# Performance work log

Measured on AMD Instinct MI355X. Metric: run time of the kernel, lower is better.

## Reference

```python
import jax, jax.numpy as jnp
import numpy as np

VOCAB = 256
UNITS = 512

def setup_inputs() -> dict:
    key = jax.random.key(0)
    ks = jax.random.split(key, 7)
    B, T = 64, 1024
    scale = 0.02
    return {
        "inputs": jax.random.randint(ks[0], (B, T), 0, VOCAB, dtype=jnp.int32),
        "emb": jax.random.normal(ks[1], (VOCAB, VOCAB), dtype=jnp.float32) * scale,
        "Wx": jax.random.normal(ks[2], (VOCAB, UNITS), dtype=jnp.float32) * scale,
        "Wh": jax.random.normal(ks[3], (UNITS, UNITS), dtype=jnp.float32) * scale,
        "b": jnp.zeros((UNITS,), dtype=jnp.float32),
        "Wd": jax.random.normal(ks[4], (UNITS, VOCAB), dtype=jnp.float32) * scale,
        "bd": jnp.zeros((VOCAB,), dtype=jnp.float32),
    }

def reference(inputs, emb, Wx, Wh, b, Wd, bd):
    # Embedding lookup: [B, T] -> [B, T, VOCAB]
    x = emb[inputs]
    B = x.shape[0]
    # Precompute input projection for all timesteps (one big GEMM)
    xp = jnp.einsum("bte,eu->btu", x, Wx) + b  # [B, T, U]
    h0 = jnp.zeros((B, Wh.shape[0]), dtype=x.dtype)

    def step(h, xp_t):
        h_new = jnp.tanh(xp_t + h @ Wh)  # SimpleRNN cell: tanh(x W_x + h W_h + b)
        return h_new, h_new

    _, hs = jax.lax.scan(step, h0, jnp.swapaxes(xp, 0, 1))  # hs: [T, B, U]
    hs = jnp.swapaxes(hs, 0, 1)  # [B, T, U]
    logits = jnp.einsum("btu,uv->btv", hs, Wd) + bd  # [B, T, VOCAB]
    return logits
```

## Files before the change

kernel.cpp:

```cpp
#include <hip/hip_runtime.h>
#include <math.h>

#define BB   64
#define TT_  1024
#define UU   512
#define VV   256
#define EE   256
#define TC   64

__device__ __forceinline__ float tanh_fast(float x) {
    float e = __expf(x + x);
    return 1.f - 2.f * __builtin_amdgcn_rcpf(e + 1.f);
}

__global__ __launch_bounds__(512) void e2_kernel(
    const float* __restrict__ emb, const float* __restrict__ Wx,
    const float* __restrict__ bias, float* __restrict__ E2)
{
    const int v = blockIdx.x;
    const int u = threadIdx.x;
    float acc = bias[u];
    const float* er = emb + v * EE;
    #pragma unroll 8
    for (int e = 0; e < EE; ++e)
        acc = fmaf(er[e], Wx[e * UU + u], acc);
    E2[v * UU + u] = acc;
}

__global__ __launch_bounds__(512, 2) void rnn_chunk_kernel(
    const int* __restrict__ toks, const float* __restrict__ E2,
    const float* __restrict__ Wh, const float* __restrict__ Wd,
    const float* __restrict__ bd,
    unsigned long long* hpub,
    float* out, int t0, int last)
{
    __shared__ float WhLDS[UU * 64];
    __shared__ float hstage[8][2][64];
    __shared__ float partials[2][8][2][64];
    __shared__ float hmine[2][2][64];
    __shared__ int   stok[2][TC];

    const int bid  = blockIdx.x;
    const int bg   = bid & 31;
    const int ug   = bid >> 5;
    const int tid  = threadIdx.x;
    const int w    = tid >> 6;
    const int lane = tid & 63;
    const int u4   = lane & 15;
    const int kq   = lane >> 4;
    const int b0   = bg * 2;

    const float4* Wh4  = (const float4*)Wh;
    float4*       WhL4 = (float4*)WhLDS;
    {
        const int col = tid & 15;
        const int kr0 = tid >> 4;
        #pragma unroll
        for (int p = 0; p < 16; ++p) {
            int k = p * 32 + kr0;
            WhL4[k * 16 + col] = Wh4[k * 128 + ug * 16 + col];
        }
    }
    if (tid < 128) {
        int b = tid >> 6, q = tid & 63;
        stok[b][q] = toks[(b0 + b) * TT_ + t0 + q];
    }
    if (t0 > 0 && tid < 128) {
        int b = tid >> 6, u = tid & 63;
        unsigned long long p =
            hpub[((size_t)((t0 - 1) & 1) * BB + (b0 + b)) * UU + ug * 64 + u];
        hmine[(t0 - 1) & 1][b][u] = __uint_as_float((unsigned int)p);
    }

    const int bmine = w & 1;
    const int vmine = (w >> 1) * 64 + lane;
    float wdreg[64];
    #pragma unroll
    for (int u = 0; u < 64; ++u)
        wdreg[u] = Wd[(ug * 64 + u) * VV + vmine];
    const float bdv = (ug == 0) ? bd[vmine] : 0.f;

    __syncthreads();

    int fails = 0;
    for (int tt = 0; tt < TC; ++tt) {
        const int s = t0 + tt;
        float xp = 0.f;
        if (w < 2) xp = E2[stok[w][tt] * UU + ug * 64 + lane];

        float acc0[4] = {0.f,0.f,0.f,0.f};
        float acc1[4] = {0.f,0.f,0.f,0.f};
        if (s > 0) {
            const int slot = (s - 1) & 1;
            const unsigned int want = (unsigned int)(s - 1);
            unsigned long long* a0 = hpub + ((size_t)slot * BB + b0) * UU + w * 64 + lane;
            unsigned long long* a1 = a0 + UU;
            unsigned long long p0 = 0, p1 = 0;
            bool got = false;
            if (fails < 3) {
                volatile const unsigned long long* f0 = a0;
                volatile const unsigned long long* f1 = a1;
                for (int it = 0; it < 24; ++it) {
                    p0 = *f0; p1 = *f1;
                    unsigned long long ok =
                        __ballot((unsigned int)(p0 >> 32) == want) &
                        __ballot((unsigned int)(p1 >> 32) == want);
                    if (ok == 0xFFFFFFFFFFFFFFFFull) { got = true; break; }
                }
                if (!got) ++fails;
            }
            if (!got) {
                while (true) {
                    p0 = __hip_atomic_load(a0, __ATOMIC_RELAXED, __HIP_MEMORY_SCOPE_AGENT);
                    p1 = __hip_atomic_load(a1, __ATOMIC_RELAXED, __HIP_MEMORY_SCOPE_AGENT);
                    unsigned long long ok =
                        __ballot((unsigned int)(p0 >> 32) == want) &
                        __ballot((unsigned int)(p1 >> 32) == want);
                    if (ok == 0xFFFFFFFFFFFFFFFFull) break;
                    __builtin_amdgcn_s_sleep(1);
                }
            }
            hstage[w][0][lane] = __uint_as_float((unsigned int)p0);
            hstage[w][1][lane] = __uint_as_float((unsigned int)p1);
            const float4* h40 = (const float4*)hstage[w][0];
            const float4* h41 = (const float4*)hstage[w][1];
            #pragma unroll
            for (int r = 0; r < 4; ++r) {
                float4 a = h40[kq * 4 + r];
                float4 c = h41[kq * 4 + r];
                float ha[4] = {a.x, a.y, a.z, a.w};
                float hc[4] = {c.x, c.y, c.z, c.w};
                #pragma unroll
                for (int q = 0; q < 4; ++q) {
                    float4 wv = WhL4[(w * 64 + kq * 16 + r * 4 + q) * 16 + u4];
                    acc0[0] = fmaf(ha[q], wv.x, acc0[0]);
                    acc0[1] = fmaf(ha[q], wv.y, acc0[1]);
                    acc0[2] = fmaf(ha[q], wv.z, acc0[2]);
                    acc0[3] = fmaf(ha[q], wv.w, acc0[3]);
                    acc1[0] = fmaf(hc[q], wv.x, acc1[0]);
                    acc1[1] = fmaf(hc[q], wv.y, acc1[1]);
                    acc1[2] = fmaf(hc[q], wv.z, acc1[2]);
                    acc1[3] = fmaf(hc[q], wv.w, acc1[3]);
                }
            }
        }

        #pragma unroll
        for (int i = 0; i < 4; ++i) {
            acc0[i] += __shfl_xor(acc0[i], 16, 64);
            acc0[i] += __shfl_xor(acc0[i], 32, 64);
            acc1[i] += __shfl_xor(acc1[i], 16, 64);
            acc1[i] += __shfl_xor(acc1[i], 32, 64);
        }
        if (kq == 0) {
            *(float4*)&partials[s & 1][w][0][u4 * 4] =
                make_float4(acc0[0], acc0[1], acc0[2], acc0[3]);
            *(float4*)&partials[s & 1][w][1][u4 * 4] =
                make_float4(acc1[0], acc1[1], acc1[2], acc1[3]);
        }
        __syncthreads();

        if (w < 2) {
            float ssum = xp;
            #pragma unroll
            for (int wv = 0; wv < 8; ++wv)
                ssum += partials[s & 1][wv][w][lane];
            float h = tanh_fast(ssum);
            unsigned long long pk =
                ((unsigned long long)(unsigned int)s << 32) | __float_as_uint(h);
            unsigned long long* dst =
                hpub + ((size_t)(s & 1) * BB + (b0 + w)) * UU + ug * 64 + lane;
            *(volatile unsigned long long*)dst = pk;
            __hip_atomic_store(dst, pk, __ATOMIC_RELAXED, __HIP_MEMORY_SCOPE_AGENT);
            hmine[s & 1][w][lane] = h;
        }

        if (s > 0) {
            const float4* hb = (const float4*)hmine[(s - 1) & 1][bmine];
            float sum = bdv;
            #pragma unroll
            for (int j = 0; j < 16; ++j) {
                float4 h4 = hb[j];
                sum = fmaf(h4.x, wdreg[4*j+0], sum);
                sum = fmaf(h4.y, wdreg[4*j+1], sum);
                sum = fmaf(h4.z, wdreg[4*j+2], sum);
                sum = fmaf(h4.w, wdreg[4*j+3], sum);
            }
            atomicAdd(out + ((size_t)(b0 + bmine) * TT_ + (s - 1)) * VV + vmine, sum);
        }
    }

    if (last) {
        __syncthreads();
        const int s = t0 + TC - 1;
        const float4* hb = (const float4*)hmine[s & 1][bmine];
        float sum = bdv;
        #pragma unroll
        for (int j = 0; j < 16; ++j) {
            float4 h4 = hb[j];
            sum = fmaf(h4.x, wdreg[4*j+0], sum);
            sum = fmaf(h4.y, wdreg[4*j+1], sum);
            sum = fmaf(h4.z, wdreg[4*j+2], sum);
            sum = fmaf(h4.w, wdreg[4*j+3], sum);
        }
        atomicAdd(out + ((size_t)(b0 + bmine) * TT_ + s) * VV + vmine, sum);
    }
}

extern "C" void kernel_launch(void* const* d_in, const int* in_sizes, int n_in,
                              void* d_out, int out_size, void* d_ws, size_t ws_size,
                              hipStream_t stream)
{
    (void)in_sizes; (void)n_in; (void)ws_size;

    const int*   toks = (const int*)  d_in[0];
    const float* emb  = (const float*)d_in[1];
    const float* Wx   = (const float*)d_in[2];
    const float* Wh   = (const float*)d_in[3];
    const float* bias = (const float*)d_in[4];
    const float* Wd   = (const float*)d_in[5];
    const float* bd   = (const float*)d_in[6];
    float* out = (float*)d_out;

    unsigned long long* hpub = (unsigned long long*)d_ws;
    float* E2 = (float*)(hpub + 2 * BB * UU);

    hipMemsetAsync(out, 0, (size_t)out_size * sizeof(float), stream);
    e2_kernel<<<EE, UU, 0, stream>>>(emb, Wx, bias, E2);

    for (int c = 0; c < TT_ / TC; ++c) {
        const int t0 = c * TC;
        rnn_chunk_kernel<<<256, 512, 0, stream>>>(
            toks, E2, Wh, Wd, bd, hpub, out, t0, c == (TT_ / TC - 1));
    }
}
```

Baseline: 2.664 ms.

## Merge RNN chunk launches into one persistent kernel with dual-scope h publishing

Result: slower. 3.225 ms (+21.1%).

```diff
diff --git a/kernel.cpp b/kernel.cpp
--- a/kernel.cpp
+++ b/kernel.cpp
@@ -6,11 +6,22 @@
 #define UU   512
 #define VV   256
 #define EE   256
-#define TC   64
+
+typedef unsigned long long u64;
 
 __device__ __forceinline__ float tanh_fast(float x) {
     float e = __expf(x + x);
     return 1.f - 2.f * __builtin_amdgcn_rcpf(e + 1.f);
+}
+
+__device__ __forceinline__ void load2_sc0(const u64* p0, const u64* p1,
+                                          u64& v0, u64& v1) {
+    asm volatile("global_load_dwordx2 %0, %2, off sc0\n\t"
+                 "global_load_dwordx2 %1, %3, off sc0\n\t"
+                 "s_waitcnt vmcnt(0)"
+                 : "=&v"(v0), "=&v"(v1)
+                 : "v"(p0), "v"(p1)
+                 : "memory");
 }
 
 __global__ __launch_bounds__(512) void e2_kernel(
@@ -27,18 +38,18 @@
     E2[v * UU + u] = acc;
 }
 
-__global__ __launch_bounds__(512, 2) void rnn_chunk_kernel(
+__global__ __launch_bounds__(512, 2) void rnn_kernel(
     const int* __restrict__ toks, const float* __restrict__ E2,
     const float* __restrict__ Wh, const float* __restrict__ Wd,
     const float* __restrict__ bd,
-    unsigned long long* hpub,
-    float* out, int t0, int last)
+    u64* hpubL, u64* hpubG,
+    float* out)
 {
     __shared__ float WhLDS[UU * 64];
     __shared__ float hstage[8][2][64];
     __shared__ float partials[2][8][2][64];
-    __shared__ float hmine[2][2][64];
-    __shared__ int   stok[2][TC];
+    __shared__ float hL[2][2][64];
+    __shared__ int   stok[2][TT_];
 
     const int bid  = blockIdx.x;
     const int bg   = bid & 31;
@@ -61,16 +72,8 @@
             WhL4[k * 16 + col] = Wh4[k * 128 + ug * 16 + col];
         }
     }
-    if (tid < 128) {
-        int b = tid >> 6, q = tid & 63;
-        stok[b][q] = toks[(b0 + b) * TT_ + t0 + q];
-    }
-    if (t0 > 0 && tid < 128) {
-        int b = tid >> 6, u = tid & 63;
-        unsigned long long p =
-            hpub[((size_t)((t0 - 1) & 1) * BB + (b0 + b)) * UU + ug * 64 + u];
-        hmine[(t0 - 1) & 1][b][u] = __uint_as_float((unsigned int)p);
-    }
+    for (int i = tid; i < 2 * TT_; i += 512)
+        stok[i >> 10][i & (TT_ - 1)] = toks[(b0 + (i >> 10)) * TT_ + (i & (TT_ - 1))];
 
     const int bmine = w & 1;
     const int vmine = (w >> 1) * 64 + lane;
@@ -82,46 +85,36 @@
 
     __syncthreads();
 
-    int fails = 0;
-    for (int tt = 0; tt < TC; ++tt) {
-        const int s = t0 + tt;
+    for (int s = 0; s < TT_; ++s) {
         float xp = 0.f;
-        if (w < 2) xp = E2[stok[w][tt] * UU + ug * 64 + lane];
+        if (w < 2) xp = E2[stok[w][s] * UU + ug * 64 + lane];
 
         float acc0[4] = {0.f,0.f,0.f,0.f};
         float acc1[4] = {0.f,0.f,0.f,0.f};
         if (s > 0) {
-            const int slot = (s - 1) & 1;
-            const unsigned int want = (unsigned int)(s - 1);
-            unsigned long long* a0 = hpub + ((size_t)slot * BB + b0) * UU + w * 64 + lane;
-            unsigned long long* a1 = a0 + UU;
-            unsigned long long p0 = 0, p1 = 0;
-            bool got = false;
-            if (fails < 3) {
-                volatile const unsigned long long* f0 = a0;
-                volatile const unsigned long long* f1 = a1;
-                for (int it = 0; it < 24; ++it) {
-                    p0 = *f0; p1 = *f1;
-                    unsigned long long ok =
-                        __ballot((unsigned int)(p0 >> 32) == want) &
-                        __ballot((unsigned int)(p1 >> 32) == want);
-                    if (ok == 0xFFFFFFFFFFFFFFFFull) { got = true; break; }
-                }
-                if (!got) ++fails;
-            }
-            if (!got) {
-                while (true) {
-                    p0 = __hip_atomic_load(a0, __ATOMIC_RELAXED, __HIP_MEMORY_SCOPE_AGENT);
-                    p1 = __hip_atomic_load(a1, __ATOMIC_RELAXED, __HIP_MEMORY_SCOPE_AGENT);
-                    unsigned long long ok =
-                        __ballot((unsigned int)(p0 >> 32) == want) &
-                        __ballot((unsigned int)(p1 >> 32) == want);
-                    if (ok == 0xFFFFFFFFFFFFFFFFull) break;
-                    __builtin_amdgcn_s_sleep(1);
+            const size_t off = ((size_t)((s - 1) & 1) * BB + b0) * UU + w * 64 + lane;
+            const u64* aL0 = hpubL + off;  const u64* aL1 = aL0 + UU;
+            const u64* aG0 = hpubG + off;  const u64* aG1 = aG0 + UU;
+            const unsigned want = (unsigned)(s - 1);
+            u64 p0 = 0, p1 = 0;
+            bool g0 = false, g1 = false;
+            int it = 0;
+            while (true) {
+                u64 t0v, t1v;
+                load2_sc0(aL0, aL1, t0v, t1v);
+                if (!g0 && (unsigned)(t0v >> 32) == want) { p0 = t0v; g0 = true; }
+                if (!g1 && (unsigned)(t1v >> 32) == want) { p1 = t1v; g1 = true; }
+                if ((__ballot(g0) & __ballot(g1)) == 0xFFFFFFFFFFFFFFFFull) break;
+                if ((++it & 3) == 0) {
+                    if (!g0) { u64 t = __hip_atomic_load(aG0, __ATOMIC_RELAXED, __HIP_MEMORY_SCOPE_AGENT);
+                               if ((unsigned)(t >> 32) == want) { p0 = t; g0 = true; } }
+                    if (!g1) { u64 t = __hip_atomic_load(aG1, __ATOMIC_RELAXED, __HIP_MEMORY_SCOPE_AGENT);
+                               if ((unsigned)(t >> 32) == want) { p1 = t; g1 = true; } }
+                    if ((__ballot(g0) & __ballot(g1)) == 0xFFFFFFFFFFFFFFFFull) break;
                 }
             }
-            hstage[w][0][lane] = __uint_as_float((unsigned int)p0);
-            hstage[w][1][lane] = __uint_as_float((unsigned int)p1);
+            hstage[w][0][lane] = __uint_as_float((unsigned)p0);
+            hstage[w][1][lane] = __uint_as_float((unsigned)p1);
             const float4* h40 = (const float4*)hstage[w][0];
             const float4* h41 = (const float4*)hstage[w][1];
             #pragma unroll
@@ -166,44 +159,42 @@
             for (int wv = 0; wv < 8; ++wv)
                 ssum += partials[s & 1][wv][w][lane];
             float h = tanh_fast(ssum);
-            unsigned long long pk =
-                ((unsigned long long)(unsigned int)s << 32) | __float_as_uint(h);
-            unsigned long long* dst =
-                hpub + ((size_t)(s & 1) * BB + (b0 + w)) * UU + ug * 64 + lane;
-            *(volatile unsigned long long*)dst = pk;
-            __hip_atomic_store(dst, pk, __ATOMIC_RELAXED, __HIP_MEMORY_SCOPE_AGENT);
-            hmine[s & 1][w][lane] = h;
+            hL[s & 1][w][lane] = h;
+            const u64 pk = ((u64)(unsigned)s << 32) | __float_as_uint(h);
+            const size_t po = ((size_t)(s & 1) * BB + (b0 + w)) * UU + ug * 64 + lane;
+            __hip_atomic_store(hpubL + po, pk, __ATOMIC_RELAXED, __HIP_MEMORY_SCOPE_WORKGROUP);
+            __hip_atomic_store(hpubG + po, pk, __ATOMIC_RELAXED, __HIP_MEMORY_SCOPE_AGENT);
         }
 
         if (s > 0) {
-            const float4* hb = (const float4*)hmine[(s - 1) & 1][bmine];
-            float sum = bdv;
+            const float4* hb = (const float4*)hL[(s - 1) & 1][bmine];
+            float lsum = bdv;
             #pragma unroll
             for (int j = 0; j < 16; ++j) {
                 float4 h4 = hb[j];
-                sum = fmaf(h4.x, wdreg[4*j+0], sum);
-                sum = fmaf(h4.y, wdreg[4*j+1], sum);
-                sum = fmaf(h4.z, wdreg[4*j+2], sum);
-                sum = fmaf(h4.w, wdreg[4*j+3], sum);
+                lsum = fmaf(h4.x, wdreg[4*j+0], lsum);
+                lsum = fmaf(h4.y, wdreg[4*j+1], lsum);
+                lsum = fmaf(h4.z, wdreg[4*j+2], lsum);
+                lsum = fmaf(h4.w, wdreg[4*j+3], lsum);
             }
-            atomicAdd(out + ((size_t)(b0 + bmine) * TT_ + (s - 1)) * VV + vmine, sum);
+            atomicAdd(out + ((size_t)(b0 + bmine) * TT_ + (s - 1)) * VV + vmine, lsum);
         }
     }
 
-    if (last) {
-        __syncthreads();
-        const int s = t0 + TC - 1;
-        const float4* hb = (const float4*)hmine[s & 1][bmine];
-        float sum = bdv;
+    __syncthreads();
+    {
+        const int s = TT_ - 1;
+        const float4* hb = (const float4*)hL[s & 1][bmine];
+        float lsum = bdv;
         #pragma unroll
         for (int j = 0; j < 16; ++j) {
             float4 h4 = hb[j];
-            sum = fmaf(h4.x, wdreg[4*j+0], sum);
-            sum = fmaf(h4.y, wdreg[4*j+1], sum);
-            sum = fmaf(h4.z, wdreg[4*j+2], sum);
-            sum = fmaf(h4.w, wdreg[4*j+3], sum);
-        }
-        atomicAdd(out + ((size_t)(b0 + bmine) * TT_ + s) * VV + vmine, sum);
+            lsum = fmaf(h4.x, wdreg[4*j+0], lsum);
+            lsum = fmaf(h4.y, wdreg[4*j+1], lsum);
+            lsum = fmaf(h4.z, wdreg[4*j+2], lsum);
+            lsum = fmaf(h4.w, wdreg[4*j+3], lsum);
+        }
+        atomicAdd(out + ((size_t)(b0 + bmine) * TT_ + s) * VV + vmine, lsum);
     }
 }
 
@@ -222,15 +213,11 @@
     const float* bd   = (const float*)d_in[6];
     float* out = (float*)d_out;
 
-    unsigned long long* hpub = (unsigned long long*)d_ws;
-    float* E2 = (float*)(hpub + 2 * BB * UU);
+    u64*   hpubL = (u64*)d_ws;
+    u64*   hpubG = hpubL + (size_t)2 * BB * UU;
+    float* E2    = (float*)(hpubG + (size_t)2 * BB * UU);
 
     hipMemsetAsync(out, 0, (size_t)out_size * sizeof(float), stream);
     e2_kernel<<<EE, UU, 0, stream>>>(emb, Wx, bias, E2);
-
-    for (int c = 0; c < TT_ / TC; ++c) {
-        const int t0 = c * TC;
-        rnn_chunk_kernel<<<256, 512, 0, stream>>>(
-            toks, E2, Wh, Wd, bd, hpub, out, t0, c == (TT_ / TC - 1));
-    }
-}
+    rnn_kernel<<<256, 512, 0, stream>>>(toks, E2, Wh, Wd, bd, hpubL, hpubG, out);
+}
```
